# Kernel optimization log

Hardware: AMD Instinct MI355X
Metric: run time of the kernel (lower is better)

Reference implementation:

```python
import jax, jax.numpy as jnp
import numpy as np

N, F, C, E = 1024, 64, 4, 32768
H = 256       # MLP hidden width
C_OUT = 4     # new edge channels produced by nn_edge


def setup_inputs() -> dict:
    key = jax.random.key(0)
    ks = jax.random.split(key, 12)
    x = jax.random.normal(ks[0], (N, F), dtype=jnp.float32)
    edge_index = jax.random.randint(ks[1], (C, 2, E), 0, N)
    edge_weight = jax.random.uniform(ks[2], (C, E), dtype=jnp.float32)
    s_n1 = 1.0 / np.sqrt(C * F)
    s_n2 = 1.0 / np.sqrt(H)
    s_e1 = 1.0 / np.sqrt(C + 2 * F)
    return {
        "x": x,
        "edge_index": edge_index,
        "edge_weight": edge_weight,
        "Wn1": jax.random.normal(ks[3], (C * F, H), dtype=jnp.float32) * s_n1,
        "bn1": jnp.zeros((H,), jnp.float32),
        "Wn2": jax.random.normal(ks[4], (H, F), dtype=jnp.float32) * s_n2,
        "bn2": jnp.zeros((F,), jnp.float32),
        "We1": jax.random.normal(ks[5], (C + 2 * F, H), dtype=jnp.float32) * s_e1,
        "be1": jnp.zeros((H,), jnp.float32),
        "We2": jax.random.normal(ks[6], (H, C_OUT), dtype=jnp.float32) * s_n2,
        "be2": jnp.zeros((C_OUT,), jnp.float32),
        "eps": jnp.zeros((), jnp.float32),
    }


def reference(x, edge_index, edge_weight, Wn1, bn1, Wn2, bn2, We1, be1, We2, be2, eps):
    # ---- MCGNN: per-channel edge-weighted scatter-add aggregation ----
    def agg_one(ei, w):
        # ei: [2,E] (row0 = source j, row1 = target i); w: [E]
        msg = x[ei[0]] * w[:, None]                       # [E,F]
        return jax.ops.segment_sum(msg, ei[1], num_segments=N)  # [N,F]

    agg = jax.vmap(agg_one)(edge_index, edge_weight)      # [C,N,F]
    out_cat = agg + (1.0 + eps) * x                       # broadcast self term
    h = out_cat.transpose(1, 0, 2).reshape(N, C * F)      # [N, C*F]
    x_next = jax.nn.relu(h @ Wn1 + bn1) @ Wn2 + bn2       # [N,F]

    # ---- EDPGNN: dense adjacency per channel + broadcast x_i/x_j ----
    def dense_adj(ei, w):
        return jnp.zeros((N, N), x.dtype).at[ei[0], ei[1]].add(w)

    a = jax.vmap(dense_adj)(edge_index, edge_weight)      # [C,N,N]
    a = a.transpose(1, 2, 0)                              # [N,N,C]
    x_i = jnp.broadcast_to(x_next[:, None, :], (N, N, F))
    x_j = jnp.broadcast_to(x_next[None, :, :], (N, N, F))
    feat = jnp.concatenate([a, x_i, x_j], axis=2).reshape(N * N, C + 2 * F)
    adj_out = (jax.nn.relu(feat @ We1 + be1) @ We2 + be2).reshape(N, N, C_OUT)
    return adj_out
```

## Files before the change

### kernel.cpp

```cpp
#include <hip/hip_runtime.h>

#define NN 1024
#define FF 64
#define CC 4
#define EE 32768
#define HH 256

#define OFF_ADENSE 0u
#define OFF_CNT    4194304u
#define OFF_OFFS   4198400u
#define OFF_CURSOR 4202512u
#define OFF_SRTS   4206608u
#define OFF_SRTW   4337680u
#define OFF_P      4468752u
#define OFF_Q      4730896u

__global__ __launch_bounds__(256)
void k_count(const int* __restrict__ ei, int* __restrict__ cnt)
{
    unsigned t = blockIdx.x * 256u + threadIdx.x;
    unsigned e = t & (EE - 1u);
    unsigned c = t >> 15;
    int dst = ei[c * 2 * EE + EE + e];
    atomicAdd(&cnt[c * NN + dst], 1);
}

__global__ __launch_bounds__(256)
void k_scan(const int* __restrict__ cnt, int* __restrict__ offs, int* __restrict__ cursor)
{
    __shared__ int wsum[4];
    const int t = threadIdx.x;
    int c[16];
    int s = 0;
    const int4* cp = (const int4*)(cnt + t * 16);
#pragma unroll
    for (int u = 0; u < 4; ++u) {
        int4 v = cp[u];
        c[u * 4 + 0] = v.x; c[u * 4 + 1] = v.y; c[u * 4 + 2] = v.z; c[u * 4 + 3] = v.w;
        s += v.x + v.y + v.z + v.w;
    }
    int incl = s;
#pragma unroll
    for (int d = 1; d < 64; d <<= 1) {
        int v = __shfl_up(incl, d, 64);
        if ((t & 63) >= d) incl += v;
    }
    const int w = t >> 6;
    if ((t & 63) == 63) wsum[w] = incl;
    __syncthreads();
    int base = incl - s;
    for (int ww = 0; ww < w; ++ww) base += wsum[ww];
    int run = base;
#pragma unroll
    for (int u = 0; u < 16; ++u) {
        offs[t * 16 + u] = run;
        cursor[t * 16 + u] = run;
        run += c[u];
    }
    if (t == 255) offs[4096] = run;
}

__global__ __launch_bounds__(256)
void k_bucket_adj(const int* __restrict__ ei, const float* __restrict__ ew,
                  int* __restrict__ cursor, int* __restrict__ srt_src,
                  float* __restrict__ srt_w, float* __restrict__ adense)
{
    unsigned t = blockIdx.x * 256u + threadIdx.x;
    unsigned e = t & (EE - 1u);
    unsigned c = t >> 15;
    int src = ei[c * 2 * EE + e];
    int dst = ei[c * 2 * EE + EE + e];
    float w = ew[c * EE + e];
    int pos = atomicAdd(&cursor[c * NN + dst], 1);
    srt_src[pos] = src;
    srt_w[pos] = w;
    atomicAdd(&adense[((size_t)src * NN + dst) * CC + c], w);
}

__global__ __launch_bounds__(1024)
void k_node(const float* __restrict__ x, const int* __restrict__ offs,
            const int* __restrict__ srt_src, const float* __restrict__ srt_w,
            const float* __restrict__ Wn1, const float* __restrict__ bn1,
            const float* __restrict__ Wn2, const float* __restrict__ bn2,
            const float* __restrict__ We1, const float* __restrict__ be1,
            const float* __restrict__ epsp,
            float* __restrict__ P, float* __restrict__ Q)
{
    __shared__ float hval[4][256];
    __shared__ float hidl[4][256];
    __shared__ float part[4][4][64];
    __shared__ float xnl[4][64];
    const int tid = threadIdx.x;
    const int n0 = blockIdx.x * 4;

    {
        const int w = tid >> 6, lane = tid & 63;
        const int c = w & 3, nn = w >> 2;
        const int g = c * NN + (n0 + nn);
        const int beg = offs[g], end = offs[g + 1];
        float acc = 0.f;
        for (int k = beg; k < end; ++k)
            acc += x[srt_src[k] * FF + lane] * srt_w[k];
        const float ope = 1.0f + epsp[0];
        hval[nn][c * 64 + lane] = acc + ope * x[(n0 + nn) * FF + lane];
    }
    __syncthreads();

    {
        const int nn = tid >> 8, h = tid & 255;
        float acc = bn1[h];
#pragma unroll 8
        for (int k = 0; k < 256; ++k)
            acc += hval[nn][k] * Wn1[k * 256 + h];
        hidl[nn][h] = fmaxf(acc, 0.f);
    }
    __syncthreads();

    {
        const int kq = tid >> 8, nn = (tid >> 6) & 3, f = tid & 63;
        float p = 0.f;
#pragma unroll 8
        for (int k = kq * 64; k < kq * 64 + 64; ++k)
            p += hidl[nn][k] * Wn2[k * 64 + f];
        part[kq][nn][f] = p;
    }
    __syncthreads();
    if (tid < 256) {
        const int nn = tid >> 6, f = tid & 63;
        xnl[nn][f] = bn2[f] + part[0][nn][f] + part[1][nn][f]
                             + part[2][nn][f] + part[3][nn][f];
    }
    __syncthreads();

    {
        const int r = tid >> 8, h = tid & 255;
        float p = be1[h], q = 0.f;
#pragma unroll 8
        for (int f = 0; f < 64; ++f) {
            float xv = xnl[r][f];
            p += xv * We1[(4 + f) * 256 + h];
            q += xv * We1[(68 + f) * 256 + h];
        }
        P[(n0 + r) * 256 + h] = p;
        Q[(n0 + r) * 256 + h] = q;
    }
}

__global__ __launch_bounds__(256, 4)
void k_edge_mlp(const float* __restrict__ P, const float* __restrict__ Q,
                const float* __restrict__ adense, const float* __restrict__ We1,
                const float* __restrict__ We2, const float* __restrict__ be2,
                float* __restrict__ out)
{
    __shared__ float4 Pl[32 * 16];
    __shared__ float4 Ql[32 * 16];

    const int tid = threadIdx.x;
    const int tx = tid & 15, ty = tid >> 4;
    const int iBase = blockIdx.y * 32, jBase = blockIdx.x * 32;
    const int psw = ty & 7;
    const int qsw = tx & 7;

    float4 a[2][2], acc[2][2];
#pragma unroll
    for (int ii = 0; ii < 2; ++ii)
#pragma unroll
        for (int jj = 0; jj < 2; ++jj) {
            a[ii][jj] = *(const float4*)(adense +
                ((size_t)(iBase + ty * 2 + ii) * NN + (jBase + tx * 2 + jj)) * 4);
            acc[ii][jj] = make_float4(0.f, 0.f, 0.f, 0.f);
        }

    for (int hc = 0; hc < 4; ++hc) {
        __syncthreads();
#pragma unroll
        for (int u = 0; u < 2; ++u) {
            int idx = tid + u * 256;
            int row = idx >> 4, q = idx & 15;
            int ph = q ^ ((row >> 1) & 7);
            Pl[row * 16 + ph] = *(const float4*)(P + (iBase + row) * 256 + hc * 64 + q * 4);
            Ql[row * 16 + ph] = *(const float4*)(Q + (jBase + row) * 256 + hc * 64 + q * 4);
        }
        __syncthreads();

        for (int q = 0; q < 16; ++q) {
            float4 w1[4], w2[4];
#pragma unroll
            for (int c = 0; c < 4; ++c)
                w1[c] = *(const float4*)(We1 + c * 256 + hc * 64 + q * 4);
#pragma unroll
            for (int k = 0; k < 4; ++k)
                w2[k] = *(const float4*)(We2 + (hc * 64 + q * 4 + k) * 4);

            float4 p[2], qv[2];
#pragma unroll
            for (int r = 0; r < 2; ++r) p[r]  = Pl[(ty * 2 + r) * 16 + (q ^ psw)];
#pragma unroll
            for (int r = 0; r < 2; ++r) qv[r] = Ql[(tx * 2 + r) * 16 + (q ^ qsw)];

#pragma unroll
            for (int ii = 0; ii < 2; ++ii) {
#pragma unroll
                for (int jj = 0; jj < 2; ++jj) {
                    const float4 av = a[ii][jj];
                    float s0 = av.x * w1[0].x + av.y * w1[1].x + av.z * w1[2].x + av.w * w1[3].x;
                    float s1 = av.x * w1[0].y + av.y * w1[1].y + av.z * w1[2].y + av.w * w1[3].y;
                    float s2 = av.x * w1[0].z + av.y * w1[1].z + av.z * w1[2].z + av.w * w1[3].z;
                    float s3 = av.x * w1[0].w + av.y * w1[1].w + av.z * w1[2].w + av.w * w1[3].w;
                    float v0 = fmaxf(p[ii].x + qv[jj].x + s0, 0.f);
                    float v1 = fmaxf(p[ii].y + qv[jj].y + s1, 0.f);
                    float v2 = fmaxf(p[ii].z + qv[jj].z + s2, 0.f);
                    float v3 = fmaxf(p[ii].w + qv[jj].w + s3, 0.f);
                    acc[ii][jj].x += v0 * w2[0].x + v1 * w2[1].x + v2 * w2[2].x + v3 * w2[3].x;
                    acc[ii][jj].y += v0 * w2[0].y + v1 * w2[1].y + v2 * w2[2].y + v3 * w2[3].y;
                    acc[ii][jj].z += v0 * w2[0].z + v1 * w2[1].z + v2 * w2[2].z + v3 * w2[3].z;
                    acc[ii][jj].w += v0 * w2[0].w + v1 * w2[1].w + v2 * w2[2].w + v3 * w2[3].w;
                }
            }
        }
    }

    const float4 b2 = *(const float4*)be2;
#pragma unroll
    for (int ii = 0; ii < 2; ++ii)
#pragma unroll
        for (int jj = 0; jj < 2; ++jj) {
            float4 o = acc[ii][jj];
            o.x += b2.x; o.y += b2.y; o.z += b2.z; o.w += b2.w;
            *(float4*)(out + ((size_t)(iBase + ty * 2 + ii) * NN + (jBase + tx * 2 + jj)) * 4) = o;
        }
}

extern "C" void kernel_launch(void* const* d_in, const int* in_sizes, int n_in,
                              void* d_out, int out_size, void* d_ws, size_t ws_size,
                              hipStream_t stream)
{
    (void)in_sizes; (void)n_in; (void)out_size; (void)ws_size;
    const float* x   = (const float*)d_in[0];
    const int*   ei  = (const int*)d_in[1];
    const float* ew  = (const float*)d_in[2];
    const float* Wn1 = (const float*)d_in[3];
    const float* bn1 = (const float*)d_in[4];
    const float* Wn2 = (const float*)d_in[5];
    const float* bn2 = (const float*)d_in[6];
    const float* We1 = (const float*)d_in[7];
    const float* be1 = (const float*)d_in[8];
    const float* We2 = (const float*)d_in[9];
    const float* be2 = (const float*)d_in[10];
    const float* eps = (const float*)d_in[11];
    float* out = (float*)d_out;

    float* ws = (float*)d_ws;
    float* adense = ws + OFF_ADENSE;
    int*   cnt    = (int*)(ws + OFF_CNT);
    int*   offs   = (int*)(ws + OFF_OFFS);
    int*   cursor = (int*)(ws + OFF_CURSOR);
    int*   srts   = (int*)(ws + OFF_SRTS);
    float* srtw   = ws + OFF_SRTW;
    float* Pb     = ws + OFF_P;
    float* Qb     = ws + OFF_Q;

    hipMemsetAsync(d_ws, 0, (size_t)(4194304 + 4096) * sizeof(float), stream);

    k_count     <<<(CC * EE) / 256, 256, 0, stream>>>(ei, cnt);
    k_scan      <<<1, 256, 0, stream>>>(cnt, offs, cursor);
    k_bucket_adj<<<(CC * EE) / 256, 256, 0, stream>>>(ei, ew, cursor, srts, srtw, adense);
    k_node      <<<NN / 4, 1024, 0, stream>>>(x, offs, srts, srtw,
                                              Wn1, bn1, Wn2, bn2, We1, be1, eps, Pb, Qb);

    dim3 g(NN / 32, NN / 32);
    k_edge_mlp<<<g, 256, 0, stream>>>(Pb, Qb, adense, We1, We2, be2, out);
}
```

Baseline: 237.3 us.

## Replace dense adjacency with tile-bucketed sparse edges and sparse ReLU correction

```diff
diff --git a/kernel.cpp b/kernel.cpp
--- a/kernel.cpp
+++ b/kernel.cpp
@@ -6,64 +6,92 @@
 #define EE 32768
 #define HH 256
 
-#define OFF_ADENSE 0u
-#define OFF_CNT    4194304u
-#define OFF_OFFS   4198400u
-#define OFF_CURSOR 4202512u
-#define OFF_SRTS   4206608u
-#define OFF_SRTW   4337680u
-#define OFF_P      4468752u
-#define OFF_Q      4730896u
+#define OFF_CNT1   0u
+#define OFF_OFFS1  4096u
+#define OFF_CUR1   8196u
+#define OFF_CNT2   12292u
+#define OFF_OFFS2  13316u
+#define OFF_CUR2   14344u
+#define OFF_SRTS   15368u
+#define OFF_SRTW   146440u
+#define OFF_TL     277512u
+#define OFF_P      539656u
+#define OFF_Q      801800u
 
 __global__ __launch_bounds__(256)
-void k_count(const int* __restrict__ ei, int* __restrict__ cnt)
+void k_count(const int* __restrict__ ei, int* __restrict__ cnt1, int* __restrict__ cnt2)
 {
     unsigned t = blockIdx.x * 256u + threadIdx.x;
     unsigned e = t & (EE - 1u);
     unsigned c = t >> 15;
+    int src = ei[c * 2 * EE + e];
     int dst = ei[c * 2 * EE + EE + e];
-    atomicAdd(&cnt[c * NN + dst], 1);
+    atomicAdd(&cnt1[c * NN + dst], 1);
+    atomicAdd(&cnt2[(src >> 5) * 32 + (dst >> 5)], 1);
 }
 
 __global__ __launch_bounds__(256)
-void k_scan(const int* __restrict__ cnt, int* __restrict__ offs, int* __restrict__ cursor)
-{
-    __shared__ int wsum[4];
+void k_scan(const int* __restrict__ cnt1, int* __restrict__ offs1, int* __restrict__ cur1,
+            const int* __restrict__ cnt2, int* __restrict__ offs2, int* __restrict__ cur2)
+{
+    __shared__ int ws1[4], ws2[4];
     const int t = threadIdx.x;
-    int c[16];
-    int s = 0;
-    const int4* cp = (const int4*)(cnt + t * 16);
-#pragma unroll
-    for (int u = 0; u < 4; ++u) {
-        int4 v = cp[u];
-        c[u * 4 + 0] = v.x; c[u * 4 + 1] = v.y; c[u * 4 + 2] = v.z; c[u * 4 + 3] = v.w;
-        s += v.x + v.y + v.z + v.w;
-    }
-    int incl = s;
-#pragma unroll
-    for (int d = 1; d < 64; d <<= 1) {
-        int v = __shfl_up(incl, d, 64);
-        if ((t & 63) >= d) incl += v;
-    }
     const int w = t >> 6;
-    if ((t & 63) == 63) wsum[w] = incl;
-    __syncthreads();
-    int base = incl - s;
-    for (int ww = 0; ww < w; ++ww) base += wsum[ww];
-    int run = base;
-#pragma unroll
-    for (int u = 0; u < 16; ++u) {
-        offs[t * 16 + u] = run;
-        cursor[t * 16 + u] = run;
-        run += c[u];
-    }
-    if (t == 255) offs[4096] = run;
+    {
+        int c[16]; int s = 0;
+        const int4* cp = (const int4*)(cnt1 + t * 16);
+#pragma unroll
+        for (int u = 0; u < 4; ++u) {
+            int4 v = cp[u];
+            c[u * 4 + 0] = v.x; c[u * 4 + 1] = v.y; c[u * 4 + 2] = v.z; c[u * 4 + 3] = v.w;
+            s += v.x + v.y + v.z + v.w;
+        }
+        int incl = s;
+#pragma unroll
+        for (int d = 1; d < 64; d <<= 1) {
+            int v = __shfl_up(incl, d, 64);
+            if ((t & 63) >= d) incl += v;
+        }
+        if ((t & 63) == 63) ws1[w] = incl;
+        __syncthreads();
+        int base = incl - s;
+        for (int ww = 0; ww < w; ++ww) base += ws1[ww];
+        int run = base;
+#pragma unroll
+        for (int u = 0; u < 16; ++u) {
+            offs1[t * 16 + u] = run;
+            cur1[t * 16 + u] = run;
+            run += c[u];
+        }
+        if (t == 255) offs1[4096] = run;
+    }
+    __syncthreads();
+    {
+        int4 v = ((const int4*)cnt2)[t];
+        int s = v.x + v.y + v.z + v.w;
+        int incl = s;
+#pragma unroll
+        for (int d = 1; d < 64; d <<= 1) {
+            int vv = __shfl_up(incl, d, 64);
+            if ((t & 63) >= d) incl += vv;
+        }
+        if ((t & 63) == 63) ws2[w] = incl;
+        __syncthreads();
+        int base = incl - s;
+        for (int ww = 0; ww < w; ++ww) base += ws2[ww];
+        offs2[t * 4]     = base;             cur2[t * 4]     = base;
+        offs2[t * 4 + 1] = base + v.x;       cur2[t * 4 + 1] = base + v.x;
+        offs2[t * 4 + 2] = base + v.x + v.y; cur2[t * 4 + 2] = base + v.x + v.y;
+        offs2[t * 4 + 3] = base + v.x + v.y + v.z;
+        cur2[t * 4 + 3]  = base + v.x + v.y + v.z;
+        if (t == 255) offs2[1024] = base + s;
+    }
 }
 
 __global__ __launch_bounds__(256)
-void k_bucket_adj(const int* __restrict__ ei, const float* __restrict__ ew,
-                  int* __restrict__ cursor, int* __restrict__ srt_src,
-                  float* __restrict__ srt_w, float* __restrict__ adense)
+void k_bucket(const int* __restrict__ ei, const float* __restrict__ ew,
+              int* __restrict__ cur1, int* __restrict__ srt_src, float* __restrict__ srt_w,
+              int* __restrict__ cur2, int2* __restrict__ tl)
 {
     unsigned t = blockIdx.x * 256u + threadIdx.x;
     unsigned e = t & (EE - 1u);
@@ -71,13 +99,14 @@
     int src = ei[c * 2 * EE + e];
     int dst = ei[c * 2 * EE + EE + e];
     float w = ew[c * EE + e];
-    int pos = atomicAdd(&cursor[c * NN + dst], 1);
-    srt_src[pos] = src;
-    srt_w[pos] = w;
-    atomicAdd(&adense[((size_t)src * NN + dst) * CC + c], w);
-}
-
-__global__ __launch_bounds__(1024)
+    int pos1 = atomicAdd(&cur1[c * NN + dst], 1);
+    srt_src[pos1] = src;
+    srt_w[pos1] = w;
+    int pos2 = atomicAdd(&cur2[(src >> 5) * 32 + (dst >> 5)], 1);
+    tl[pos2] = make_int2((src << 12) | (dst << 2) | (int)c, __float_as_int(w));
+}
+
+__global__ __launch_bounds__(512)
 void k_node(const float* __restrict__ x, const int* __restrict__ offs,
             const int* __restrict__ srt_src, const float* __restrict__ srt_w,
             const float* __restrict__ Wn1, const float* __restrict__ bn1,
@@ -86,12 +115,12 @@
             const float* __restrict__ epsp,
             float* __restrict__ P, float* __restrict__ Q)
 {
-    __shared__ float hval[4][256];
-    __shared__ float hidl[4][256];
-    __shared__ float part[4][4][64];
-    __shared__ float xnl[4][64];
+    __shared__ float hval[2][256];
+    __shared__ float hidl[2][256];
+    __shared__ float part[4][2][64];
+    __shared__ float xnl[2][64];
     const int tid = threadIdx.x;
-    const int n0 = blockIdx.x * 4;
+    const int n0 = blockIdx.x * 2;
 
     {
         const int w = tid >> 6, lane = tid & 63;
@@ -117,7 +146,7 @@
     __syncthreads();
 
     {
-        const int kq = tid >> 8, nn = (tid >> 6) & 3, f = tid & 63;
+        const int kq = tid >> 7, nn = (tid >> 6) & 1, f = tid & 63;
         float p = 0.f;
 #pragma unroll 8
         for (int k = kq * 64; k < kq * 64 + 64; ++k)
@@ -125,7 +154,7 @@
         part[kq][nn][f] = p;
     }
     __syncthreads();
-    if (tid < 256) {
+    if (tid < 128) {
         const int nn = tid >> 6, f = tid & 63;
         xnl[nn][f] = bn2[f] + part[0][nn][f] + part[1][nn][f]
                              + part[2][nn][f] + part[3][nn][f];
@@ -146,33 +175,66 @@
     }
 }
 
-__global__ __launch_bounds__(256, 4)
+__global__ __launch_bounds__(256, 3)
 void k_edge_mlp(const float* __restrict__ P, const float* __restrict__ Q,
-                const float* __restrict__ adense, const float* __restrict__ We1,
-                const float* __restrict__ We2, const float* __restrict__ be2,
-                float* __restrict__ out)
-{
+                const int* __restrict__ toffs, const int2* __restrict__ tl,
+                const float* __restrict__ We1, const float* __restrict__ We2,
+                const float* __restrict__ be2, float* __restrict__ out)
+{
+    __shared__ float4 aT[32 * 32];
+    __shared__ float4 corr[32 * 32];
     __shared__ float4 Pl[32 * 16];
     __shared__ float4 Ql[32 * 16];
+    __shared__ unsigned short list[1024];
+    __shared__ int nList;
 
     const int tid = threadIdx.x;
+    const int bi = blockIdx.y, bj = blockIdx.x;
+    const int iBase = bi * 32, jBase = bj * 32;
+    const int tile = bi * 32 + bj;
+
+#pragma unroll
+    for (int u = 0; u < 4; ++u) {
+        aT[tid + u * 256]   = make_float4(0.f, 0.f, 0.f, 0.f);
+        corr[tid + u * 256] = make_float4(0.f, 0.f, 0.f, 0.f);
+    }
+    if (tid == 0) nList = 0;
+    __syncthreads();
+
+    {
+        const int beg = toffs[tile], n = toffs[tile + 1] - beg;
+        float* aTf = (float*)aT;
+        for (int k = tid; k < n; k += 256) {
+            int2 ent = tl[beg + k];
+            int li = (ent.x >> 12) & 31, lj = (ent.x >> 2) & 31, c = ent.x & 3;
+            atomicAdd(&aTf[(li * 32 + lj) * 4 + c], __int_as_float(ent.y));
+        }
+    }
+    __syncthreads();
+
+#pragma unroll
+    for (int u = 0; u < 4; ++u) {
+        int p = tid * 4 + u;
+        float4 a4 = aT[p];
+        if (a4.x != 0.f || a4.y != 0.f || a4.z != 0.f || a4.w != 0.f) {
+            int idx = atomicAdd(&nList, 1);
+            list[idx] = (unsigned short)p;
+        }
+    }
+    __syncthreads();
+    const int nL = nList;
+
     const int tx = tid & 15, ty = tid >> 4;
-    const int iBase = blockIdx.y * 32, jBase = blockIdx.x * 32;
-    const int psw = ty & 7;
-    const int qsw = tx & 7;
-
-    float4 a[2][2], acc[2][2];
+    const int psw = ty & 7, qsw = tx & 7;
+
+    float4 acc[2][2];
 #pragma unroll
     for (int ii = 0; ii < 2; ++ii)
 #pragma unroll
-        for (int jj = 0; jj < 2; ++jj) {
-            a[ii][jj] = *(const float4*)(adense +
-                ((size_t)(iBase + ty * 2 + ii) * NN + (jBase + tx * 2 + jj)) * 4);
+        for (int jj = 0; jj < 2; ++jj)
             acc[ii][jj] = make_float4(0.f, 0.f, 0.f, 0.f);
-        }
 
     for (int hc = 0; hc < 4; ++hc) {
-        __syncthreads();
 #pragma unroll
         for (int u = 0; u < 2; ++u) {
             int idx = tid + u * 256;
@@ -183,34 +245,25 @@
         }
         __syncthreads();
 
+#pragma unroll 4
         for (int q = 0; q < 16; ++q) {
-            float4 w1[4], w2[4];
-#pragma unroll
-            for (int c = 0; c < 4; ++c)
-                w1[c] = *(const float4*)(We1 + c * 256 + hc * 64 + q * 4);
+            float4 w2[4];
 #pragma unroll
             for (int k = 0; k < 4; ++k)
                 w2[k] = *(const float4*)(We2 + (hc * 64 + q * 4 + k) * 4);
-
             float4 p[2], qv[2];
 #pragma unroll
             for (int r = 0; r < 2; ++r) p[r]  = Pl[(ty * 2 + r) * 16 + (q ^ psw)];
 #pragma unroll
             for (int r = 0; r < 2; ++r) qv[r] = Ql[(tx * 2 + r) * 16 + (q ^ qsw)];
-
 #pragma unroll
             for (int ii = 0; ii < 2; ++ii) {
 #pragma unroll
                 for (int jj = 0; jj < 2; ++jj) {
-                    const float4 av = a[ii][jj];
-                    float s0 = av.x * w1[0].x + av.y * w1[1].x + av.z * w1[2].x + av.w * w1[3].x;
-                    float s1 = av.x * w1[0].y + av.y * w1[1].y + av.z * w1[2].y + av.w * w1[3].y;
-                    float s2 = av.x * w1[0].z + av.y * w1[1].z + av.z * w1[2].z + av.w * w1[3].z;
-                    float s3 = av.x * w1[0].w + av.y * w1[1].w + av.z * w1[2].w + av.w * w1[3].w;
-                    float v0 = fmaxf(p[ii].x + qv[jj].x + s0, 0.f);
-                    float v1 = fmaxf(p[ii].y + qv[jj].y + s1, 0.f);
-                    float v2 = fmaxf(p[ii].z + qv[jj].z + s2, 0.f);
-                    float v3 = fmaxf(p[ii].w + qv[jj].w + s3, 0.f);
+                    float v0 = fmaxf(p[ii].x + qv[jj].x, 0.f);
+                    float v1 = fmaxf(p[ii].y + qv[jj].y, 0.f);
+                    float v2 = fmaxf(p[ii].z + qv[jj].z, 0.f);
+                    float v3 = fmaxf(p[ii].w + qv[jj].w, 0.f);
                     acc[ii][jj].x += v0 * w2[0].x + v1 * w2[1].x + v2 * w2[2].x + v3 * w2[3].x;
                     acc[ii][jj].y += v0 * w2[0].y + v1 * w2[1].y + v2 * w2[2].y + v3 * w2[3].y;
                     acc[ii][jj].z += v0 * w2[0].z + v1 * w2[1].z + v2 * w2[2].z + v3 * w2[3].z;
@@ -218,6 +271,41 @@
                 }
             }
         }
+
+        for (int en = tid; en < nL; en += 256) {
+            int p = list[en];
+            int li = p >> 5, lj = p & 31;
+            float4 a4 = aT[p];
+            float4 cc = corr[p];
+            const int ps2 = (li >> 1) & 7, qs2 = (lj >> 1) & 7;
+#pragma unroll 4
+            for (int q = 0; q < 16; ++q) {
+                float4 w1[4], w2[4];
+#pragma unroll
+                for (int c = 0; c < 4; ++c)
+                    w1[c] = *(const float4*)(We1 + c * 256 + hc * 64 + q * 4);
+#pragma unroll
+                for (int k = 0; k < 4; ++k)
+                    w2[k] = *(const float4*)(We2 + (hc * 64 + q * 4 + k) * 4);
+                float4 pv = Pl[li * 16 + (q ^ ps2)];
+                float4 qv = Ql[lj * 16 + (q ^ qs2)];
+                float s0 = a4.x * w1[0].x + a4.y * w1[1].x + a4.z * w1[2].x + a4.w * w1[3].x;
+                float s1 = a4.x * w1[0].y + a4.y * w1[1].y + a4.z * w1[2].y + a4.w * w1[3].y;
+                float s2 = a4.x * w1[0].z + a4.y * w1[1].z + a4.z * w1[2].z + a4.w * w1[3].z;
+                float s3 = a4.x * w1[0].w + a4.y * w1[1].w + a4.z * w1[2].w + a4.w * w1[3].w;
+                float b0 = pv.x + qv.x, b1 = pv.y + qv.y, b2_ = pv.z + qv.z, b3 = pv.w + qv.w;
+                float d0 = fmaxf(b0 + s0, 0.f) - fmaxf(b0, 0.f);
+                float d1 = fmaxf(b1 + s1, 0.f) - fmaxf(b1, 0.f);
+                float d2 = fmaxf(b2_ + s2, 0.f) - fmaxf(b2_, 0.f);
+                float d3 = fmaxf(b3 + s3, 0.f) - fmaxf(b3, 0.f);
+                cc.x += d0 * w2[0].x + d1 * w2[1].x + d2 * w2[2].x + d3 * w2[3].x;
+                cc.y += d0 * w2[0].y + d1 * w2[1].y + d2 * w2[2].y + d3 * w2[3].y;
+                cc.z += d0 * w2[0].z + d1 * w2[1].z + d2 * w2[2].z + d3 * w2[3].z;
+                cc.w += d0 * w2[0].w + d1 * w2[1].w + d2 * w2[2].w + d3 * w2[3].w;
+            }
+            corr[p] = cc;
+        }
+        __syncthreads();
     }
 
     const float4 b2 = *(const float4*)be2;
@@ -225,8 +313,11 @@
     for (int ii = 0; ii < 2; ++ii)
 #pragma unroll
         for (int jj = 0; jj < 2; ++jj) {
+            int p = (ty * 2 + ii) * 32 + (tx * 2 + jj);
+            float4 cr = corr[p];
             float4 o = acc[ii][jj];
-            o.x += b2.x; o.y += b2.y; o.z += b2.z; o.w += b2.w;
+            o.x += b2.x + cr.x; o.y += b2.y + cr.y;
+            o.z += b2.z + cr.z; o.w += b2.w + cr.w;
             *(float4*)(out + ((size_t)(iBase + ty * 2 + ii) * NN + (jBase + tx * 2 + jj)) * 4) = o;
         }
 }
@@ -251,23 +342,26 @@
     float* out = (float*)d_out;
 
     float* ws = (float*)d_ws;
-    float* adense = ws + OFF_ADENSE;
-    int*   cnt    = (int*)(ws + OFF_CNT);
-    int*   offs   = (int*)(ws + OFF_OFFS);
-    int*   cursor = (int*)(ws + OFF_CURSOR);
-    int*   srts   = (int*)(ws + OFF_SRTS);
-    float* srtw   = ws + OFF_SRTW;
-    float* Pb     = ws + OFF_P;
-    float* Qb     = ws + OFF_Q;
-
-    hipMemsetAsync(d_ws, 0, (size_t)(4194304 + 4096) * sizeof(float), stream);
-
-    k_count     <<<(CC * EE) / 256, 256, 0, stream>>>(ei, cnt);
-    k_scan      <<<1, 256, 0, stream>>>(cnt, offs, cursor);
-    k_bucket_adj<<<(CC * EE) / 256, 256, 0, stream>>>(ei, ew, cursor, srts, srtw, adense);
-    k_node      <<<NN / 4, 1024, 0, stream>>>(x, offs, srts, srtw,
-                                              Wn1, bn1, Wn2, bn2, We1, be1, eps, Pb, Qb);
+    int*   cnt1  = (int*)(ws + OFF_CNT1);
+    int*   offs1 = (int*)(ws + OFF_OFFS1);
+    int*   cur1  = (int*)(ws + OFF_CUR1);
+    int*   cnt2  = (int*)(ws + OFF_CNT2);
+    int*   offs2 = (int*)(ws + OFF_OFFS2);
+    int*   cur2  = (int*)(ws + OFF_CUR2);
+    int*   srts  = (int*)(ws + OFF_SRTS);
+    float* srtw  = ws + OFF_SRTW;
+    int2*  tl    = (int2*)(ws + OFF_TL);
+    float* Pb    = ws + OFF_P;
+    float* Qb    = ws + OFF_Q;
+
+    hipMemsetAsync(d_ws, 0, (size_t)13316 * sizeof(int), stream);
+
+    k_count <<<(CC * EE) / 256, 256, 0, stream>>>(ei, cnt1, cnt2);
+    k_scan  <<<1, 256, 0, stream>>>(cnt1, offs1, cur1, cnt2, offs2, cur2);
+    k_bucket<<<(CC * EE) / 256, 256, 0, stream>>>(ei, ew, cur1, srts, srtw, cur2, tl);
+    k_node  <<<NN / 2, 512, 0, stream>>>(x, offs1, srts, srtw,
+                                         Wn1, bn1, Wn2, bn2, We1, be1, eps, Pb, Qb);
 
     dim3 g(NN / 32, NN / 32);
-    k_edge_mlp<<<g, 256, 0, stream>>>(Pb, Qb, adense, We1, We2, be2, out);
-}
+    k_edge_mlp<<<g, 256, 0, stream>>>(Pb, Qb, offs2, tl, We1, We2, be2, out);
+}
```

New measurement: 250.8 us. 1.06x slower.
